# Kernel tuning notes

Measured on AMD Instinct MI355X. Metric: run time of the kernel, lower is better.

## Reference

```python
import jax, jax.numpy as jnp
import numpy as np

HIDDEN = 1024
HEADS = 16
HEAD_DIM = HIDDEN // HEADS  # 64
MAX_SEQ = 2048


def _rope_tables():
    # RotaryEmbedding buffers: freqs_cos/sin of shape [max_seq_len, head_dim//2]
    inv_freq = 1.0 / (10000.0 ** (jnp.arange(0, HEAD_DIM, 2, dtype=jnp.float32) / HEAD_DIM))
    t = jnp.arange(MAX_SEQ, dtype=jnp.float32)
    freqs = t[:, None] * inv_freq[None, :]
    return jnp.cos(freqs), jnp.sin(freqs)


def setup_inputs() -> dict:
    key = jax.random.key(0)
    k1, k2, k3 = jax.random.split(key, 3)
    x = jax.random.normal(k1, (2, 2048, HIDDEN), dtype=jnp.float32)
    qkv_w = jax.random.normal(k2, (HIDDEN, 3 * HIDDEN), dtype=jnp.float32) * 0.02
    qkv_b = jnp.zeros((3 * HIDDEN,), dtype=jnp.float32)
    out_w = jax.random.normal(k3, (HIDDEN, HIDDEN), dtype=jnp.float32) * 0.02
    out_b = jnp.zeros((HIDDEN,), dtype=jnp.float32)
    return {"x": x, "qkv_w": qkv_w, "qkv_b": qkv_b, "out_w": out_w, "out_b": out_b}


def reference(x, qkv_w, qkv_b, out_w, out_b):
    b, s, _ = x.shape
    qkv = x @ qkv_w + qkv_b                                   # [b, s, 3*hidden]
    qkv = qkv.reshape(b, s, HEADS, 3 * HEAD_DIM).transpose(0, 2, 1, 3)  # [b, h, s, 3*hd]
    q, k, v = jnp.split(qkv, 3, axis=-1)                      # each [b, h, s, hd]

    # Faithful to source quirk: rotary() is called on [b, h, s, hd] tensors so
    # x.shape[1] == num_heads -> seq_pos = arange(num_heads); tables are indexed
    # by HEAD index and broadcast over the sequence axis.
    cos_tab, sin_tab = _rope_tables()
    cos = cos_tab[:HEADS][None, :, None, :]                   # [1, h, 1, hd/2]
    sin = sin_tab[:HEADS][None, :, None, :]

    def rot(u):
        u1 = u[..., : HEAD_DIM // 2]
        u2 = u[..., HEAD_DIM // 2 :]
        return jnp.concatenate([u1 * cos - u2 * sin, u2 * cos + u1 * sin], axis=-1)

    q = rot(q)
    k = rot(k)

    scores = jnp.einsum("bhqd,bhkd->bhqk", q, k) / (HEAD_DIM ** 0.5)  # [b, h, s, s]
    attn = jax.nn.softmax(scores.astype(jnp.float32), axis=-1).astype(scores.dtype)
    out = jnp.einsum("bhqk,bhkd->bhqd", attn, v)              # [b, h, s, hd]
    out = out.transpose(0, 2, 1, 3).reshape(b, s, HEADS * HEAD_DIM)
    return out @ out_w + out_b
```

## Files before the change

### kernel.cpp

```cpp
#include <hip/hip_runtime.h>
#include <hip/hip_bf16.h>
#include <cstdint>
#include <cstddef>

typedef float  f32x4  __attribute__((ext_vector_type(4)));
typedef __bf16 bf16x8 __attribute__((ext_vector_type(8)));
typedef __bf16 bf16x4 __attribute__((ext_vector_type(4)));

#define HIDDEN 1024
#define SEQ    2048
#define BATCH  2
#define NQKV   3072
#define MTOT   4096

__device__ __forceinline__ __bf16 f2bf(float f) {
  unsigned u = __builtin_bit_cast(unsigned, f);
  u += 0x7FFFu + ((u >> 16) & 1u);
  unsigned short s = (unsigned short)(u >> 16);
  return __builtin_bit_cast(__bf16, s);
}

__device__ __forceinline__ unsigned pk2(float a, float b) {
  unsigned ua = __builtin_bit_cast(unsigned, a) + 0x8000u;
  unsigned ub = __builtin_bit_cast(unsigned, b) + 0x8000u;
  return __builtin_amdgcn_perm(ub, ua, 0x07060302u);
}

__device__ __forceinline__ float fexp2(float x) {
#if __has_builtin(__builtin_amdgcn_exp2f)
  return __builtin_amdgcn_exp2f(x);
#else
  return exp2f(x);
#endif
}

__device__ __forceinline__ void async16(const void* g, void* l) {
  __builtin_amdgcn_global_load_lds((__attribute__((address_space(1))) void*)(g),
                                   (__attribute__((address_space(3))) void*)(l),
                                   16, 0, 0);
}

__global__ __launch_bounds__(256) void k_prep(const float* __restrict__ x,
                                              __bf16* __restrict__ xb,
                                              const float* __restrict__ qkv_w,
                                              __bf16* __restrict__ wqkT,
                                              const float* __restrict__ out_w,
                                              __bf16* __restrict__ woT) {
  __shared__ float tile[64][65];
  const int bid = blockIdx.x, t = threadIdx.x;
  if (bid < 4096) {
    int i = bid * 256 + t;
    float4 v = ((const float4*)x)[i];
    bf16x4 o;
    o[0] = f2bf(v.x); o[1] = f2bf(v.y); o[2] = f2bf(v.z); o[3] = f2bf(v.w);
    ((bf16x4*)xb)[i] = o;
    return;
  }
  const float* W; __bf16* WT; int N, bx, by;
  if (bid < 4864) { int g = bid - 4096; W = qkv_w; WT = wqkT; N = NQKV;  bx = g % 48; by = g / 48; }
  else            { int g = bid - 4864; W = out_w; WT = woT;  N = HIDDEN; bx = g % 16; by = g / 16; }
  const int K = HIDDEN;
  int tx = t & 63, ty = t >> 6;
  int n0 = bx * 64, k0 = by * 64;
#pragma unroll
  for (int r = 0; r < 16; r++) {
    int row = r * 4 + ty;
    tile[row][tx] = W[(size_t)(k0 + row) * N + n0 + tx];
  }
  __syncthreads();
#pragma unroll
  for (int i2 = 0; i2 < 2; i2++) {
    int cc = i2 * 256 + t;
    int n = cc >> 3, ch = cc & 7;
    bf16x8 o;
#pragma unroll
    for (int j = 0; j < 8; j++) o[j] = f2bf(tile[ch * 8 + j][n]);
    *(bf16x8*)(WT + (size_t)(n0 + n) * K + k0 + ch * 8) = o;
  }
}

__global__ __launch_bounds__(512, 2) void k_qkv(const __bf16* __restrict__ A,
                                                const __bf16* __restrict__ BT,
                                                const float* __restrict__ bias,
                                                __bf16* __restrict__ Cout,
                                                __bf16* __restrict__ vt) {
  const int K = HIDDEN;
  __shared__ __align__(16) __bf16 As[4][256 * 32];
  __shared__ __align__(16) __bf16 Bs[4][256 * 32];
  const int t = threadIdx.x;
  const int lane = t & 63, wv = t >> 6;
  const int ln = lane & 15, quad = lane >> 4;
  const int sw8 = (quad ^ ((ln >> 1) & 3)) * 8;
  const int wm = (wv >> 2) * 128, wn = (wv & 3) * 64;

  const int lin = blockIdx.x;
  const int xcd = lin & 7, wi = lin >> 3;
  const int bxi = (xcd & 3) * 3 + wi % 3;
  const int byi = (xcd >> 2) * 8 + wi / 3;
  const int m0 = byi * 256, n0 = bxi * 256;

  auto stage = [&](int k0, int p) {
    __bf16* Ad = As[p];
    __bf16* Bd = Bs[p];
#pragma unroll
    for (int i = 0; i < 2; i++) {
      int tt = i * 512 + t;
      int row = tt >> 2, ch = tt & 3;
      int chs = ch ^ ((row >> 1) & 3);
      async16(A + (size_t)(m0 + row) * K + k0 + chs * 8, Ad + tt * 8);
    }
#pragma unroll
    for (int i = 0; i < 2; i++) {
      int tt = i * 512 + t;
      int row = tt >> 2, ch = tt & 3;
      int chs = ch ^ ((row >> 1) & 3);
      async16(BT + (size_t)(n0 + row) * K + k0 + chs * 8, Bd + tt * 8);
    }
  };

  const f32x4 zero4 = {0.f, 0.f, 0.f, 0.f};
  f32x4 acc[8][4];
#pragma unroll
  for (int i = 0; i < 8; i++)
#pragma unroll
    for (int j = 0; j < 4; j++) acc[i][j] = zero4;

  stage(0, 0); stage(32, 1); stage(64, 2);
  const int NIT = K / 32;
  for (int j = 0; j < NIT; j++) {
    int rem = NIT - 1 - j;
    if (rem >= 2)      asm volatile("s_waitcnt vmcnt(8)\n\ts_barrier" ::: "memory");
    else if (rem == 1) asm volatile("s_waitcnt vmcnt(4)\n\ts_barrier" ::: "memory");
    else               asm volatile("s_waitcnt vmcnt(0)\n\ts_barrier" ::: "memory");
    if (j + 3 < NIT) stage((j + 3) * 32, (j + 3) & 3);
    const __bf16* Asb = As[j & 3];
    const __bf16* Bsb = Bs[j & 3];
    bf16x8 af[8], bfr[4];
#pragma unroll
    for (int x = 0; x < 8; x++)
      af[x] = *(const bf16x8*)(Asb + (wm + x * 16 + ln) * 32 + sw8);
#pragma unroll
    for (int x = 0; x < 4; x++)
      bfr[x] = *(const bf16x8*)(Bsb + (wn + x * 16 + ln) * 32 + sw8);
#pragma unroll
    for (int mt = 0; mt < 8; mt++)
#pragma unroll
      for (int nt = 0; nt < 4; nt++)
        acc[mt][nt] = __builtin_amdgcn_mfma_f32_16x16x32_bf16(af[mt], bfr[nt], acc[mt][nt], 0, 0, 0);
  }

  const float CE = 0.125f * 1.44269504089f;
#pragma unroll
  for (int nt = 0; nt < 4; nt++) {
    int g = n0 + wn + nt * 16;
    int col = g + ln;
    float bv = bias[col];
    int off = g % 192;
    if (off < 128) {
      float scl = (off < 64) ? CE : 1.0f;
#pragma unroll
      for (int mt = 0; mt < 8; mt++) {
#pragma unroll
        for (int r = 0; r < 4; r++) {
          int row = m0 + wm + mt * 16 + quad * 4 + r;
          Cout[(size_t)row * NQKV + col] = f2bf((acc[mt][nt][r] + bv) * scl);
        }
      }
    } else {
      int hg = g / 192;
      int d  = off - 128 + ln;
#pragma unroll
      for (int mt = 0; mt < 8; mt++) {
        int rowb = m0 + wm + mt * 16;
        int bb = rowb >> 11;
        int s  = rowb & 2047;
        int sblk = s >> 7;
        int blk  = (s >> 4) & 7;
        int p = (blk & 3) * 32 + quad * 8 + ((blk >> 2) << 2);
        uint2 o;
        o.x = pk2(acc[mt][nt][0] + bv, acc[mt][nt][1] + bv);
        o.y = pk2(acc[mt][nt][2] + bv, acc[mt][nt][3] + bv);
        *(uint2*)(vt + ((size_t)((bb * 16 + hg) * 64 + d)) * SEQ + sblk * 128 + p) = o;
      }
    }
  }
}

__global__ __launch_bounds__(256, 4) void k_gemm_out(const __bf16* __restrict__ A,
                                                     const __bf16* __restrict__ BT,
                                                     const float* __restrict__ bias,
                                                     float* __restrict__ Cout,
                                                     int M, int N, int K) {
  constexpr int TN = 64;
  __shared__ __align__(16) __bf16 As[2 * 128 * 32];
  __shared__ __align__(16) __bf16 Bs[2 * TN * 32];
  const int t = threadIdx.x;
  const int lane = t & 63, wv = t >> 6;
  const int ln = lane & 15, quad = lane >> 4;
  const int sw8 = (quad ^ ((ln >> 1) & 3)) * 8;
  const int wm = (wv & 1) * 64, wn = (wv >> 1) * (TN / 2);

  const int nbx = N / TN;
  const int cx = nbx >> 1;
  const int lin = blockIdx.x;
  const int xcd = lin & 7, wi = lin >> 3;
  const int bxi = (xcd & 1) * cx + wi % cx;
  const int byi = (xcd >> 1) * 8 + wi / cx;
  const int m0 = byi * 128, n0 = bxi * TN;

  auto stage = [&](int k0, int p) {
    __bf16* Ad = As + p * (128 * 32);
    __bf16* Bd = Bs + p * (TN * 32);
#pragma unroll
    for (int i = 0; i < 2; i++) {
      int tt = i * 256 + t;
      int row = tt >> 2, ch = tt & 3;
      int chs = ch ^ ((row >> 1) & 3);
      async16(A + (size_t)(m0 + row) * K + k0 + chs * 8, Ad + tt * 8);
    }
    {
      int tt = t;
      int row = tt >> 2, ch = tt & 3;
      int chs = ch ^ ((row >> 1) & 3);
      async16(BT + (size_t)(n0 + row) * K + k0 + chs * 8, Bd + tt * 8);
    }
  };

  const f32x4 zero4 = {0.f, 0.f, 0.f, 0.f};
  f32x4 acc[4][2];
#pragma unroll
  for (int i = 0; i < 4; i++)
#pragma unroll
    for (int j = 0; j < 2; j++) acc[i][j] = zero4;

  stage(0, 0);
  const int NIT = K / 32;
  for (int it = 0; it < NIT; it++) {
    __syncthreads();
    if (it + 1 < NIT) stage((it + 1) * 32, (it + 1) & 1);
    const __bf16* Asb = As + (it & 1) * (128 * 32);
    const __bf16* Bsb = Bs + (it & 1) * (TN * 32);
    bf16x8 af[4], bfr[2];
#pragma unroll
    for (int x = 0; x < 4; x++)
      af[x] = *(const bf16x8*)(Asb + (wm + x * 16 + ln) * 32 + sw8);
#pragma unroll
    for (int x = 0; x < 2; x++)
      bfr[x] = *(const bf16x8*)(Bsb + (wn + x * 16 + ln) * 32 + sw8);
#pragma unroll
    for (int mt = 0; mt < 4; mt++)
#pragma unroll
      for (int nt = 0; nt < 2; nt++)
        acc[mt][nt] = __builtin_amdgcn_mfma_f32_16x16x32_bf16(af[mt], bfr[nt], acc[mt][nt], 0, 0, 0);
  }
#pragma unroll
  for (int nt = 0; nt < 2; nt++) {
    int col = n0 + wn + nt * 16 + ln;
    float bv = bias[col];
#pragma unroll
    for (int mt = 0; mt < 4; mt++) {
#pragma unroll
      for (int r = 0; r < 4; r++) {
        int row = m0 + wm + mt * 16 + quad * 4 + r;
        Cout[(size_t)row * N + col] = acc[mt][nt][r] + bv;
      }
    }
  }
}

__global__ __launch_bounds__(512, 4) void k_attn(const __bf16* __restrict__ qkv,
                                                 const __bf16* __restrict__ vt,
                                                 __bf16* __restrict__ aout) {
  __shared__ __align__(16) __bf16 smem[32768];
  const int t = threadIdx.x;
  const int lane = t & 63, wv = t >> 6;
  const int ln = lane & 15, quad = lane >> 4;
  const int sw8 = (quad ^ ((ln >> 1) & 3)) * 8;

  int gid = blockIdx.x;
  int slot = gid & 7, j = gid >> 3;
  int bh = slot * 4 + (j >> 4);
  int qt0 = j & 15;
  const int b = bh >> 4, h = bh & 15;
  const int q0 = qt0 * 128;

  const __bf16* qbase = qkv + (size_t)b * SEQ * NQKV + h * 192;
  const __bf16* kbase = qbase + 64;
  const __bf16* vbase = vt + (size_t)bh * 64 * SEQ;

#pragma unroll
  for (int i = 0; i < 2; i++) {
    int tt = i * 512 + t;
    int hh = tt >> 9, row = (tt >> 2) & 127, ch = tt & 3;
    int chs = ch ^ ((row >> 1) & 3);
    async16(kbase + (size_t)row * NQKV + hh * 32 + chs * 8, smem + tt * 8);
  }
#pragma unroll
  for (int i = 0; i < 2; i++) {
    int tt = i * 512 + t;
    int c = tt >> 8, d = (tt >> 2) & 63, w = tt & 3;
    int ws = w ^ ((d >> 1) & 3);
    async16(vbase + (size_t)d * SEQ + c * 32 + ws * 8, smem + 16384 + tt * 8);
  }

  bf16x8 qf[2];
#pragma unroll
  for (int dc = 0; dc < 2; dc++)
    qf[dc] = *(const bf16x8*)(qbase + (size_t)(q0 + wv * 16 + ln) * NQKV + dc * 32 + quad * 8);

  union { unsigned u[4]; bf16x8 v; } ones;
  ones.u[0] = ones.u[1] = ones.u[2] = ones.u[3] = 0x3F803F80u;

  const f32x4 zero4 = {0.f, 0.f, 0.f, 0.f};
  f32x4 O[4];
  f32x4 Ol = zero4;
#pragma unroll
  for (int dt = 0; dt < 4; dt++) O[dt] = zero4;

  for (int it = 0; it < SEQ / 128; it++) {
    __syncthreads();
    const __bf16* Ks = smem + (it & 1) * 8192;
    const __bf16* Vs = smem + 16384 + (it & 1) * 8192;
    if (it + 1 < SEQ / 128) {
      __bf16* Kd = smem + ((it + 1) & 1) * 8192;
      __bf16* Vd = smem + 16384 + ((it + 1) & 1) * 8192;
      const __bf16* kn = kbase + (size_t)(it + 1) * 128 * NQKV;
      const __bf16* vn = vbase + (it + 1) * 128;
#pragma unroll
      for (int i = 0; i < 2; i++) {
        int tt = i * 512 + t;
        int hh = tt >> 9, row = (tt >> 2) & 127, ch = tt & 3;
        int chs = ch ^ ((row >> 1) & 3);
        async16(kn + (size_t)row * NQKV + hh * 32 + chs * 8, Kd + tt * 8);
      }
#pragma unroll
      for (int i = 0; i < 2; i++) {
        int tt = i * 512 + t;
        int c = tt >> 8, d = (tt >> 2) & 63, w = tt & 3;
        int ws = w ^ ((d >> 1) & 3);
        async16(vn + (size_t)d * SEQ + c * 32 + ws * 8, Vd + tt * 8);
      }
    }

    unsigned Pp[8][2];
#pragma unroll
    for (int blk = 0; blk < 8; blk++) {
      bf16x8 kf0 = *(const bf16x8*)(Ks +        (blk * 16 + ln) * 32 + sw8);
      bf16x8 kf1 = *(const bf16x8*)(Ks + 4096 + (blk * 16 + ln) * 32 + sw8);
      __builtin_amdgcn_s_setprio(1);
      f32x4 s = __builtin_amdgcn_mfma_f32_16x16x32_bf16(kf0, qf[0], zero4, 0, 0, 0);
      s = __builtin_amdgcn_mfma_f32_16x16x32_bf16(kf1, qf[1], s, 0, 0, 0);
      __builtin_amdgcn_s_setprio(0);
      Pp[blk][0] = pk2(fexp2(s[0]), fexp2(s[1]));
      Pp[blk][1] = pk2(fexp2(s[2]), fexp2(s[3]));
    }
#pragma unroll
    for (int kc = 0; kc < 4; kc++) {
      union { bf16x8 v; unsigned u[4]; } pf;
      pf.u[0] = Pp[kc][0]; pf.u[1] = Pp[kc][1];
      pf.u[2] = Pp[kc + 4][0]; pf.u[3] = Pp[kc + 4][1];
      __builtin_amdgcn_s_setprio(1);
      Ol = __builtin_amdgcn_mfma_f32_16x16x32_bf16(pf.v, ones.v, Ol, 0, 0, 0);
#pragma unroll
      for (int dt = 0; dt < 4; dt++) {
        bf16x8 vf = *(const bf16x8*)(Vs + kc * 2048 + (dt * 16 + ln) * 32 + sw8);
        O[dt] = __builtin_amdgcn_mfma_f32_16x16x32_bf16(pf.v, vf, O[dt], 0, 0, 0);
      }
      __builtin_amdgcn_s_setprio(0);
    }
  }

  __bf16* stage = smem + wv * 1024;
#pragma unroll
  for (int r = 0; r < 4; r++) {
    float ir = 1.0f / Ol[r];
#pragma unroll
    for (int dt = 0; dt < 4; dt++)
      stage[(quad * 4 + r) * 64 + dt * 16 + ln] = f2bf(O[dt][r] * ir);
  }
  __bf16* obase = aout + (size_t)(b * SEQ + q0 + wv * 16) * HIDDEN + h * 64;
#pragma unroll
  for (int i = 0; i < 2; i++) {
    int tt = i * 64 + lane; int row = tt >> 3, ch = tt & 7;
    *(bf16x8*)(obase + (size_t)row * HIDDEN + ch * 8) = *(const bf16x8*)(stage + row * 64 + ch * 8);
  }
}

extern "C" void kernel_launch(void* const* d_in, const int* in_sizes, int n_in,
                              void* d_out, int out_size, void* d_ws, size_t ws_size,
                              hipStream_t stream) {
  const float* x     = (const float*)d_in[0];
  const float* qkv_w = (const float*)d_in[1];
  const float* qkv_b = (const float*)d_in[2];
  const float* out_w = (const float*)d_in[3];
  const float* out_b = (const float*)d_in[4];

  char* ws = (char*)d_ws;
  __bf16* xb   = (__bf16*)(ws);
  __bf16* wqkT = (__bf16*)(ws + 8388608);
  __bf16* woT  = (__bf16*)(ws + 14680064);
  __bf16* qkv  = (__bf16*)(ws + 16777216);
  __bf16* vt   = (__bf16*)(ws + 41943040);
  __bf16* aout = (__bf16*)(ws + 50331648);

  k_prep<<<5120, 256, 0, stream>>>(x, xb, qkv_w, wqkT, out_w, woT);
  k_qkv<<<192, 512, 0, stream>>>(xb, wqkT, qkv_b, qkv, vt);
  k_attn<<<512, 512, 0, stream>>>(qkv, vt, aout);
  k_gemm_out<<<512, 256, 0, stream>>>(aout, woT, out_b, (float*)d_out, MTOT, HIDDEN, HIDDEN);
}
```

Baseline: 188.1 us.

## Restructure QKV GEMM main loop into four-phase ping-pong schedule with K=64 tiles

Rewrites the k_qkv main loop to use K=64 tiles split into two 128-row halves, double-buffered in LDS, with a new XOR swizzle over 8 chunks. Each K-step is divided into four phases, each loading a quarter of the fragments, issuing one async stage of the next tiles, then running its MFMA batch between barriers with raised priority. The aim is to overlap global-to-LDS traffic and LDS reads with MFMA work and cut per-iteration barrier and waitcnt overhead. It adds many more barriers per step and a tricky vmcnt accounting, which could stall or be mis-synchronised. The other kernels only switch to an MFMA macro.

```diff
diff --git a/kernel.cpp b/kernel.cpp
--- a/kernel.cpp
+++ b/kernel.cpp
@@ -39,6 +39,8 @@
                                    (__attribute__((address_space(3))) void*)(l),
                                    16, 0, 0);
 }
+
+#define MFMA16(a, b, c) __builtin_amdgcn_mfma_f32_16x16x32_bf16((a), (b), (c), 0, 0, 0)
 
 __global__ __launch_bounds__(256) void k_prep(const float* __restrict__ x,
                                               __bf16* __restrict__ xb,
@@ -85,12 +87,11 @@
                                                 __bf16* __restrict__ Cout,
                                                 __bf16* __restrict__ vt) {
   const int K = HIDDEN;
-  __shared__ __align__(16) __bf16 As[4][256 * 32];
-  __shared__ __align__(16) __bf16 Bs[4][256 * 32];
+  __shared__ __align__(16) __bf16 As[2][2][8192];
+  __shared__ __align__(16) __bf16 Bs[2][2][8192];
   const int t = threadIdx.x;
   const int lane = t & 63, wv = t >> 6;
   const int ln = lane & 15, quad = lane >> 4;
-  const int sw8 = (quad ^ ((ln >> 1) & 3)) * 8;
   const int wm = (wv >> 2) * 128, wn = (wv & 3) * 64;
 
   const int lin = blockIdx.x;
@@ -99,22 +100,26 @@
   const int byi = (xcd >> 2) * 8 + wi / 3;
   const int m0 = byi * 256, n0 = bxi * 256;
 
-  auto stage = [&](int k0, int p) {
-    __bf16* Ad = As[p];
-    __bf16* Bd = Bs[p];
+  auto stA = [&](int kt, int h) {
+    __bf16* dst = &As[kt & 1][h][0];
+    const __bf16* src = A + (size_t)m0 * K + kt * 64;
 #pragma unroll
     for (int i = 0; i < 2; i++) {
       int tt = i * 512 + t;
-      int row = tt >> 2, ch = tt & 3;
-      int chs = ch ^ ((row >> 1) & 3);
-      async16(A + (size_t)(m0 + row) * K + k0 + chs * 8, Ad + tt * 8);
-    }
+      int sr = tt >> 3, ch = tt & 7;
+      int gr = (sr & 63) + ((sr >> 6) << 7) + h * 64;
+      async16(src + (size_t)gr * K + ((ch ^ (sr & 7)) * 8), dst + tt * 8);
+    }
+  };
+  auto stB = [&](int kt, int h) {
+    __bf16* dst = &Bs[kt & 1][h][0];
+    const __bf16* src = BT + (size_t)n0 * K + kt * 64;
 #pragma unroll
     for (int i = 0; i < 2; i++) {
       int tt = i * 512 + t;
-      int row = tt >> 2, ch = tt & 3;
-      int chs = ch ^ ((row >> 1) & 3);
-      async16(BT + (size_t)(n0 + row) * K + k0 + chs * 8, Bd + tt * 8);
+      int sr = tt >> 3, ch = tt & 7;
+      int gr = (sr & 63) + ((sr >> 6) << 7) + h * 64;
+      async16(src + (size_t)gr * K + ((ch ^ (sr & 7)) * 8), dst + tt * 8);
     }
   };
 
@@ -125,28 +130,103 @@
 #pragma unroll
     for (int j = 0; j < 4; j++) acc[i][j] = zero4;
 
-  stage(0, 0); stage(32, 1); stage(64, 2);
-  const int NIT = K / 32;
-  for (int j = 0; j < NIT; j++) {
-    int rem = NIT - 1 - j;
-    if (rem >= 2)      asm volatile("s_waitcnt vmcnt(8)\n\ts_barrier" ::: "memory");
-    else if (rem == 1) asm volatile("s_waitcnt vmcnt(4)\n\ts_barrier" ::: "memory");
-    else               asm volatile("s_waitcnt vmcnt(0)\n\ts_barrier" ::: "memory");
-    if (j + 3 < NIT) stage((j + 3) * 32, (j + 3) & 3);
-    const __bf16* Asb = As[j & 3];
-    const __bf16* Bsb = Bs[j & 3];
-    bf16x8 af[8], bfr[4];
-#pragma unroll
-    for (int x = 0; x < 8; x++)
-      af[x] = *(const bf16x8*)(Asb + (wm + x * 16 + ln) * 32 + sw8);
-#pragma unroll
-    for (int x = 0; x < 4; x++)
-      bfr[x] = *(const bf16x8*)(Bsb + (wn + x * 16 + ln) * 32 + sw8);
-#pragma unroll
-    for (int mt = 0; mt < 8; mt++)
-#pragma unroll
-      for (int nt = 0; nt < 4; nt++)
-        acc[mt][nt] = __builtin_amdgcn_mfma_f32_16x16x32_bf16(af[mt], bfr[nt], acc[mt][nt], 0, 0, 0);
+  stA(0, 0); stA(0, 1); stB(0, 0); stB(0, 1);
+  stA(1, 0); stB(1, 0); stB(1, 1);
+
+  bf16x8 af[4][2], bf[4][2];
+  const int sra = ln + ((wv >> 2) << 6);
+  const int scb = ln + (((wv & 3) >> 1) << 6);
+  const int swz = ln & 7;
+
+  const int NT = K / 64;
+  for (int kt = 0; kt < NT; kt++) {
+    const int p = kt & 1;
+    if (kt < NT - 1) asm volatile("s_waitcnt vmcnt(6)" ::: "memory");
+    else             asm volatile("s_waitcnt vmcnt(0)" ::: "memory");
+    __builtin_amdgcn_s_barrier();
+    const __bf16* Bh = &Bs[p][wv & 1][0];
+    {
+      const __bf16* Ah = &As[p][0][0];
+#pragma unroll
+      for (int m = 0; m < 4; m++)
+#pragma unroll
+        for (int kk = 0; kk < 2; kk++)
+          af[m][kk] = *(const bf16x8*)(Ah + (sra + m * 16) * 64 + (((kk * 4 + quad) ^ swz) * 8));
+#pragma unroll
+      for (int n = 0; n < 2; n++)
+#pragma unroll
+        for (int kk = 0; kk < 2; kk++)
+          bf[n][kk] = *(const bf16x8*)(Bh + (scb + n * 16) * 64 + (((kk * 4 + quad) ^ swz) * 8));
+      if (kt + 1 < NT) stA(kt + 1, 1);
+      __builtin_amdgcn_s_barrier();
+      asm volatile("s_waitcnt lgkmcnt(0)" ::: "memory");
+      __builtin_amdgcn_sched_barrier(0);
+      __builtin_amdgcn_s_setprio(1);
+#pragma unroll
+      for (int m = 0; m < 4; m++)
+#pragma unroll
+        for (int n = 0; n < 2; n++) {
+          acc[m][n] = MFMA16(af[m][0], bf[n][0], acc[m][n]);
+          acc[m][n] = MFMA16(af[m][1], bf[n][1], acc[m][n]);
+        }
+      __builtin_amdgcn_s_setprio(0);
+      __builtin_amdgcn_s_barrier();
+    }
+    {
+#pragma unroll
+      for (int n = 2; n < 4; n++)
+#pragma unroll
+        for (int kk = 0; kk < 2; kk++)
+          bf[n][kk] = *(const bf16x8*)(Bh + (scb + n * 16) * 64 + (((kk * 4 + quad) ^ swz) * 8));
+      if (kt + 2 < NT) stA(kt + 2, 0);
+      __builtin_amdgcn_s_barrier();
+      asm volatile("s_waitcnt lgkmcnt(0)" ::: "memory");
+      __builtin_amdgcn_sched_barrier(0);
+      __builtin_amdgcn_s_setprio(1);
+#pragma unroll
+      for (int m = 0; m < 4; m++)
+#pragma unroll
+        for (int n = 2; n < 4; n++) {
+          acc[m][n] = MFMA16(af[m][0], bf[n][0], acc[m][n]);
+          acc[m][n] = MFMA16(af[m][1], bf[n][1], acc[m][n]);
+        }
+      __builtin_amdgcn_s_setprio(0);
+      __builtin_amdgcn_s_barrier();
+    }
+    {
+      const __bf16* Ah = &As[p][1][0];
+#pragma unroll
+      for (int m = 0; m < 4; m++)
+#pragma unroll
+        for (int kk = 0; kk < 2; kk++)
+          af[m][kk] = *(const bf16x8*)(Ah + (sra + m * 16) * 64 + (((kk * 4 + quad) ^ swz) * 8));
+      if (kt + 2 < NT) stB(kt + 2, 0);
+      __builtin_amdgcn_s_barrier();
+      asm volatile("s_waitcnt lgkmcnt(0)" ::: "memory");
+      __builtin_amdgcn_sched_barrier(0);
+      __builtin_amdgcn_s_setprio(1);
+#pragma unroll
+      for (int m = 0; m < 4; m++)
+#pragma unroll
+        for (int n = 2; n < 4; n++) {
+          acc[4 + m][n] = MFMA16(af[m][0], bf[n][0], acc[4 + m][n]);
+          acc[4 + m][n] = MFMA16(af[m][1], bf[n][1], acc[4 + m][n]);
+        }
+      __builtin_amdgcn_s_setprio(0);
+      __builtin_amdgcn_s_barrier();
+    }
+    {
+      if (kt + 2 < NT) stB(kt + 2, 1);
+      __builtin_amdgcn_s_setprio(1);
+#pragma unroll
+      for (int m = 0; m < 4; m++)
+#pragma unroll
+        for (int n = 0; n < 2; n++) {
+          acc[4 + m][n] = MFMA16(af[m][0], bf[n][0], acc[4 + m][n]);
+          acc[4 + m][n] = MFMA16(af[m][1], bf[n][1], acc[4 + m][n]);
+        }
+      __builtin_amdgcn_s_setprio(0);
+    }
   }
 
   const float CE = 0.125f * 1.44269504089f;
@@ -176,11 +256,11 @@
         int s  = rowb & 2047;
         int sblk = s >> 7;
         int blk  = (s >> 4) & 7;
-        int p = (blk & 3) * 32 + quad * 8 + ((blk >> 2) << 2);
+        int pp = (blk & 3) * 32 + quad * 8 + ((blk >> 2) << 2);
         uint2 o;
         o.x = pk2(acc[mt][nt][0] + bv, acc[mt][nt][1] + bv);
         o.y = pk2(acc[mt][nt][2] + bv, acc[mt][nt][3] + bv);
-        *(uint2*)(vt + ((size_t)((bb * 16 + hg) * 64 + d)) * SEQ + sblk * 128 + p) = o;
+        *(uint2*)(vt + ((size_t)((bb * 16 + hg) * 64 + d)) * SEQ + sblk * 128 + pp) = o;
       }
     }
   }
@@ -251,7 +331,7 @@
     for (int mt = 0; mt < 4; mt++)
 #pragma unroll
       for (int nt = 0; nt < 2; nt++)
-        acc[mt][nt] = __builtin_amdgcn_mfma_f32_16x16x32_bf16(af[mt], bfr[nt], acc[mt][nt], 0, 0, 0);
+        acc[mt][nt] = MFMA16(af[mt], bfr[nt], acc[mt][nt]);
   }
 #pragma unroll
   for (int nt = 0; nt < 2; nt++) {
@@ -348,8 +428,8 @@
       bf16x8 kf0 = *(const bf16x8*)(Ks +        (blk * 16 + ln) * 32 + sw8);
       bf16x8 kf1 = *(const bf16x8*)(Ks + 4096 + (blk * 16 + ln) * 32 + sw8);
       __builtin_amdgcn_s_setprio(1);
-      f32x4 s = __builtin_amdgcn_mfma_f32_16x16x32_bf16(kf0, qf[0], zero4, 0, 0, 0);
-      s = __builtin_amdgcn_mfma_f32_16x16x32_bf16(kf1, qf[1], s, 0, 0, 0);
+      f32x4 s = MFMA16(kf0, qf[0], zero4);
+      s = MFMA16(kf1, qf[1], s);
       __builtin_amdgcn_s_setprio(0);
       Pp[blk][0] = pk2(fexp2(s[0]), fexp2(s[1]));
       Pp[blk][1] = pk2(fexp2(s[2]), fexp2(s[3]));
@@ -360,11 +440,11 @@
       pf.u[0] = Pp[kc][0]; pf.u[1] = Pp[kc][1];
       pf.u[2] = Pp[kc + 4][0]; pf.u[3] = Pp[kc + 4][1];
       __builtin_amdgcn_s_setprio(1);
-      Ol = __builtin_amdgcn_mfma_f32_16x16x32_bf16(pf.v, ones.v, Ol, 0, 0, 0);
+      Ol = MFMA16(pf.v, ones.v, Ol);
 #pragma unroll
       for (int dt = 0; dt < 4; dt++) {
         bf16x8 vf = *(const bf16x8*)(Vs + kc * 2048 + (dt * 16 + ln) * 32 + sw8);
-        O[dt] = __builtin_amdgcn_mfma_f32_16x16x32_bf16(pf.v, vf, O[dt], 0, 0, 0);
+        O[dt] = MFMA16(pf.v, vf, O[dt]);
       }
       __builtin_amdgcn_s_setprio(0);
     }
```

Result: faster. 178.8 us (-5.0%).
